# Kernel optimization log

Hardware: AMD Instinct MI355X
Metric: run time of the kernel (lower is better)

Reference implementation:

```python
import jax, jax.numpy as jnp
import numpy as np

N, C, T, V, O, S, R = 32, 64, 256, 25, 192, 3, 8  # batch, in_ch, time, joints, out_ch, subsets, rel_ch


def setup_inputs() -> dict:
    key = jax.random.key(0)
    ks = jax.random.split(key, 20)
    w = lambda i, shape: (jax.random.normal(ks[i], shape, jnp.float32) * 0.05)
    return {
        "x": jax.random.normal(ks[0], (N, C, T, V), jnp.float32),
        "spd_A": jax.random.normal(ks[1], (V, V), jnp.float32) * 0.1,
        "A3": jax.random.normal(ks[2], (S, V, V), jnp.float32) * 0.1,
        "A6": jax.random.normal(ks[3], (6, V, V), jnp.float32) * 0.1,
        "conv1_w": w(4, (S, R, C)), "conv1_b": jnp.zeros((S, R), jnp.float32),
        "conv2_w": w(5, (S, R, C)), "conv2_b": jnp.zeros((S, R), jnp.float32),
        "conv4_w": w(6, (S, O, R)), "conv4_b": jnp.zeros((S, O), jnp.float32),
        "conv3_w": w(7, (S, O, C)), "conv3_b": jnp.zeros((S, O), jnp.float32),
        "alpha": jnp.full((1,), 0.5, jnp.float32),
        "beta": jnp.full((1,), 0.5, jnp.float32),
        "gamma": jnp.full((1,), 0.5, jnp.float32),
        "bn_w": jnp.ones((O,), jnp.float32), "bn_b": jnp.zeros((O,), jnp.float32),
        "down_w": w(8, (O, C)), "down_b": jnp.zeros((O,), jnp.float32),
        "dbn_w": jnp.ones((O,), jnp.float32), "dbn_b": jnp.zeros((O,), jnp.float32),
    }


def _bn(y, w, b):
    # BatchNorm2d in training mode: stats over (N, T, V) per channel, biased var
    mu = y.mean(axis=(0, 2, 3), keepdims=True)
    var = ((y - mu) ** 2).mean(axis=(0, 2, 3), keepdims=True)
    return (y - mu) * jax.lax.rsqrt(var + 1e-5) * w[None, :, None, None] + b[None, :, None, None]


def reference(x, spd_A, A3, A6, conv1_w, conv1_b, conv2_w, conv2_b, conv4_w, conv4_b,
              conv3_w, conv3_b, alpha, beta, gamma, bn_w, bn_b, down_w, down_b, dbn_w, dbn_b):
    out_c = conv4_w.shape[1]
    # A6 expanded: (out//6, 6, V, V) -> (out, V, V); contiguous-view == tile along channel blocks
    A6_ex = jnp.tile(A6, (out_c // 6, 1, 1))  # (O, V, V)
    # 1x1 conv then temporal mean == conv on temporal mean (linear op commutes)
    xm = x.mean(axis=2)  # (N, C, V)
    x1 = jnp.einsum('ncv,src->nsrv', xm, conv1_w) + conv1_b[None, :, :, None]
    x2 = jnp.einsum('ncv,src->nsrv', xm, conv2_w) + conv2_b[None, :, :, None]
    d = jnp.tanh(x1[..., :, None] - x2[..., None, :])  # (N, S, R, V, V)
    A_dyn = jnp.einsum('nsruv,sor->nsouv', d, conv4_w) + conv4_b[None, :, :, None, None]
    A_at = (A_dyn * alpha + A3[None, :, None, :, :]
            + A6_ex[None, None] * beta + spd_A[None, None, None] * gamma)  # (N, S, O, V, V)
    # CTRGC_2: x3 = conv3(x); einsum 'ncuv,nctv->nctu', summed over subsets
    x3 = jnp.einsum('nctv,soc->nsotv', x, conv3_w) + conv3_b[None, :, :, None, None]
    y = jnp.einsum('nsouv,nsotv->notu', A_at, x3)  # (N, O, T, V)
    y = _bn(y, bn_w, bn_b)
    xd = jnp.einsum('nctv,oc->notv', x, down_w) + down_b[None, :, None, None]
    y = jax.nn.relu(y + _bn(xd, dbn_w, dbn_b))
    return y
```

## Files before the change

### kernel.cpp

```cpp
#include <hip/hip_runtime.h>

#define N_ 32
#define C_ 64
#define T_ 256
#define V_ 25
#define O_ 192
#define S_ 3
#define R_ 8
#define VV (V_*V_)
#define TV (T_*V_)
#define RP 26
#define TRP (T_*RP)

typedef unsigned short u16;
typedef unsigned int u32;
typedef __attribute__((ext_vector_type(4))) u16 u16x4;
typedef __attribute__((ext_vector_type(8))) u16 u16x8;
typedef __attribute__((ext_vector_type(4))) u32 u32x4;
typedef __attribute__((ext_vector_type(8))) __bf16 bf16x8;
typedef __attribute__((ext_vector_type(4))) float f32x4;

#define WS_A2F_U 0
#define WS_XQ_U  (18874368)
#define WS_XD_U  (18874368 + 13631488)
#define WS_XM_F   (35913728)
#define WS_RS_F   (35913728 + 51200)
#define WS_STAT_F (35913728 + 51200 + 153600)
#define WS_COEF_F (35913728 + 51200 + 153600 + 768)

__device__ __forceinline__ u16 f2b(float f) {
    return __builtin_bit_cast(u16, (__bf16)f);
}
__device__ __forceinline__ float b2f(u16 u) {
    return __builtin_bit_cast(float, ((unsigned)u) << 16);
}
__device__ __forceinline__ f32x4 mfma16(bf16x8 a, bf16x8 b, f32x4 c) {
    return __builtin_amdgcn_mfma_f32_16x16x32_bf16(a, b, c, 0, 0, 0);
}

__global__ void k0_xq(const float* __restrict__ x, u16* __restrict__ xq) {
    __shared__ float tile[64][52];
    int bid = blockIdx.x;
    int n = bid >> 7, tb = bid & 127;
    int t0 = tb * 2;
    int tid = threadIdx.x;
    const float2* xp = (const float2*)(x + (size_t)n * C_ * TV + t0 * 25);
    for (int p = tid; p < 1600; p += 256) {
        int c = p / 25, q = p % 25;
        float2 f2 = xp[(size_t)c * 3200 + q];
        tile[c][q * 2] = f2.x;
        tile[c][q * 2 + 1] = f2.y;
    }
    __syncthreads();
    for (int p = tid; p < 832; p += 256) {
        int row = p >> 4, c4g = p & 15;
        int t = row >= RP, v = row - t * RP;
        u16x4 w;
        #pragma unroll
        for (int i = 0; i < 4; ++i) {
            int co = ((c4g & 3) << 4) + ((c4g >> 2) << 2) + i;
            w[i] = (v < 25) ? f2b(tile[co][t * 25 + v]) : (u16)0;
        }
        *(u16x4*)&xq[((size_t)n * TRP + tb * 52 + row) * 64 + c4g * 4] = w;
    }
}

__global__ void k1_xm(const float* __restrict__ x, float* __restrict__ xm_out) {
    __shared__ float ps[256];
    int nc = blockIdx.x;
    int tid = threadIdx.x;
    const float* xp = x + (size_t)nc * TV;
    float acc = 0.f;
    if (tid < 250) {
        int tg = tid / 25, v = tid % 25;
        for (int j = 0; j < 26; ++j) {
            int t = tg + 10 * j;
            if (t < T_) acc += xp[t * V_ + v];
        }
    }
    ps[tid] = acc;
    __syncthreads();
    if (tid < V_) {
        float s = 0.f;
        for (int tg = 0; tg < 10; ++tg) s += ps[tg * 25 + tid];
        xm_out[(size_t)nc * V_ + tid] = s * (1.f / T_);
    }
}

__global__ void k2_a2f(const float* __restrict__ spd, const float* __restrict__ A3,
                       const float* __restrict__ A6,
                       const float* __restrict__ w1, const float* __restrict__ b1,
                       const float* __restrict__ w2, const float* __restrict__ b2,
                       const float* __restrict__ w4, const float* __restrict__ b4,
                       const float* __restrict__ b3,
                       const float* __restrict__ alpha, const float* __restrict__ beta,
                       const float* __restrict__ gamma,
                       u16* __restrict__ a2f, const float* __restrict__ xmbuf,
                       float* __restrict__ rs_tot) {
    __shared__ float xm[C_ * V_];
    __shared__ float x1s[R_ * V_], x2s[R_ * V_];
    __shared__ float dm[R_ * VV];
    __shared__ float a3s[VV], sps[VV], a6s[6 * VV];
    __shared__ float aat[2 * VV];
    __shared__ float w4s[2][R_];
    __shared__ float b4s[2];
    int bid = blockIdx.x;
    int n = bid / 24;
    int rem = bid % 24;
    int s = rem / 8, og = rem % 8;
    int tid = threadIdx.x;
    const float* xmg = xmbuf + (size_t)n * C_ * V_;
    for (int p = tid; p < C_ * V_; p += 256) xm[p] = xmg[p];
    for (int p = tid; p < VV; p += 256) { a3s[p] = A3[s * VV + p]; sps[p] = spd[p]; }
    for (int p = tid; p < 6 * VV; p += 256) a6s[p] = A6[p];
    __syncthreads();
    if (tid < R_ * V_) {
        int r = tid / V_, v = tid % V_;
        float acc1 = b1[s * R_ + r], acc2 = b2[s * R_ + r];
        for (int c = 0; c < C_; ++c) {
            float xv = xm[c * V_ + v];
            acc1 += xv * w1[(s * R_ + r) * C_ + c];
            acc2 += xv * w2[(s * R_ + r) * C_ + c];
        }
        x1s[tid] = acc1; x2s[tid] = acc2;
    }
    __syncthreads();
    for (int p = tid; p < R_ * VV; p += 256) {
        int r = p / VV, uv = p % VV, u = uv / V_, v = uv % V_;
        dm[p] = tanhf(x1s[r * V_ + u] - x2s[r * V_ + v]);
    }
    __syncthreads();
    float al = alpha[0], be = beta[0], ga = gamma[0];
    for (int op = 0; op < 12; ++op) {
        int o0 = og * 24 + op * 2;
        if (tid < 16) w4s[tid >> 3][tid & 7] =
            w4[((size_t)(s * O_ + o0 + (tid >> 3))) * R_ + (tid & 7)];
        if (tid < 2) b4s[tid] = b4[s * O_ + o0 + tid];
        __syncthreads();
        for (int p = tid; p < 2 * VV; p += 256) {
            int oo = p / VV, pp = p % VV;
            float acc = b4s[oo];
            #pragma unroll
            for (int r = 0; r < R_; ++r) acc += dm[r * VV + pp] * w4s[oo][r];
            int o = o0 + oo;
            aat[p] = al * acc + a3s[pp] + be * a6s[(o % 6) * VV + pp] + ga * sps[pp];
        }
        __syncthreads();
        if (tid < 2 * V_) {
            int oo = tid / V_, u = tid % V_;
            float rs = 0.f;
            for (int v = 0; v < V_; ++v) rs += aat[oo * VV + u * V_ + v];
            atomicAdd(&rs_tot[((size_t)(n * O_ + o0 + oo)) * V_ + u],
                      b3[s * O_ + o0 + oo] * rs);
        }
        {
            int oo = tid >> 7, l2 = tid & 127, cu = l2 >> 6, l = l2 & 63;
            int u = cu * 16 + (l & 15);
            u16x8 w;
            #pragma unroll
            for (int j = 0; j < 8; ++j) {
                int v = ((j >> 2) << 4) + ((l >> 4) << 2) + (j & 3);
                float val = 0.f;
                if (u < V_ && v < V_) val = aat[oo * VV + u * V_ + v];
                w[j] = f2b(val);
            }
            size_t idx = ((((size_t)(n * O_ + o0 + oo)) * S_ + s) * 2 + cu) * 64 + l;
            ((u16x8*)a2f)[idx] = w;
        }
        __syncthreads();
    }
}

#define OSTR_B 2504
#define SSTR_B 832
#define BUF_B  20096

__global__ __launch_bounds__(256, 3)
void k3_main(const u16* __restrict__ xq,
             const float* __restrict__ w3, const float* __restrict__ dw,
             const float* __restrict__ db,
             const u16* __restrict__ a2f, const float* __restrict__ rs_tot,
             float* __restrict__ yout, u16* __restrict__ xdws,
             float* __restrict__ stats) {
    __shared__ char x3Lb[2 * BUF_B];
    int orig = blockIdx.x;
    int bid = (orig & 7) * 96 + (orig >> 3);
    int n = bid / 24;
    int o0 = (bid % 24) * 8;
    int tid = threadIdx.x, wid = tid >> 6, lane = tid & 63;
    int lr = lane & 15, lg = lane >> 4;
    int colt = wid & 1;
    int rt0 = (wid >> 1) * 13;

    for (int p = tid; p < 2 * BUF_B / 16; p += 256) ((u32x4*)x3Lb)[p] = u32x4{0,0,0,0};

    const float* wsrc = (colt == 0)
        ? w3 + ((size_t)((lr >> 3) * O_ + o0 + (lr & 7))) * C_
        : ((lr < 8) ? w3 + ((size_t)(2 * O_ + o0 + lr)) * C_
                    : dw + ((size_t)(o0 + lr - 8)) * C_);
    bf16x8 bw[2];
    #pragma unroll
    for (int ks = 0; ks < 2; ++ks) {
        u16x8 tmp;
        #pragma unroll
        for (int j = 0; j < 8; ++j) {
            int c = ks * 32 + (lg << 2) + (j & 3) + ((j >> 2) << 4);
            tmp[j] = f2b(wsrc[c]);
        }
        bw[ks] = __builtin_bit_cast(bf16x8, tmp);
    }
    float dbv = (colt == 1 && lr >= 8) ? db[o0 + lr - 8] : 0.f;

    int wo = (colt == 0) ? (lr & 7) : lr;
    int wsb = (colt == 0) ? (lr >> 3) : 2;
    int colbyte = wo * OSTR_B + wsb * SSTR_B;

    const bf16x8* a2v = (const bf16x8*)a2f;
    bf16x8 Bh[2][6];
    float rsb0[2], rsb1[2];
    #pragma unroll
    for (int oi = 0; oi < 2; ++oi) {
        int o = o0 + (wid << 1) + oi;
        const bf16x8* bp = a2v + ((size_t)(n * O_ + o)) * 6 * 64 + lane;
        #pragma unroll
        for (int q = 0; q < 6; ++q) Bh[oi][q] = bp[(size_t)q * 64];
        const float* rsp = rs_tot + ((size_t)(n * O_ + o)) * V_;
        rsb0[oi] = rsp[lr];
        rsb1[oi] = (lr < 9) ? rsp[16 + lr] : 0.f;
    }

    float sy1[2] = {0, 0}, sy2[2] = {0, 0};
    float sd1 = 0.f, sd2 = 0.f;
    const u16* xbn = xq + (size_t)n * TRP * 64;
    int rdw = 13 * lr + 2 * lg;
    __syncthreads();

    for (int ch = 0; ch < 16; ++ch) {
        int t0 = ch * 16;
        char* buf = x3Lb + (ch & 1) * BUF_B;
        const u16* xrow = xbn + (size_t)t0 * RP * 64;
        for (int rt = rt0; rt < rt0 + 13; ++rt) {
            const u16* ap = xrow + (size_t)(rt * 16 + lr) * 64 + (lg << 4);
            u16x8 A0 = *(const u16x8*)ap;
            u16x8 A1 = *(const u16x8*)(ap + 8);
            f32x4 acc = {0.f, 0.f, 0.f, 0.f};
            acc = mfma16(__builtin_bit_cast(bf16x8, A0), bw[0], acc);
            acc = mfma16(__builtin_bit_cast(bf16x8, A1), bw[1], acc);
            int rbase = rt * 16 + (lg << 2);
            if (colt == 0 || lr < 8) {
                u16x4 w;
                #pragma unroll
                for (int reg = 0; reg < 4; ++reg) w[reg] = f2b(acc[reg]);
                *(u16x4*)(buf + colbyte + rbase * 2) = w;
            } else {
                size_t xdb = ((size_t)(n * O_ + o0 + lr - 8)) * TV + (size_t)t0 * V_;
                #pragma unroll
                for (int reg = 0; reg < 4; ++reg) {
                    int rr = rbase + reg;
                    int t = rr / RP, v = rr - t * RP;
                    if (v < 25) {
                        float val = acc[reg] + dbv;
                        xdws[xdb + t * V_ + v] = f2b(val);
                        sd1 += val; sd2 += val * val;
                    }
                }
            }
        }
        __syncthreads();
        #pragma unroll
        for (int oi = 0; oi < 2; ++oi) {
            int ol = (wid << 1) + oi;
            int o = o0 + ol;
            const u32* L = (const u32*)(buf + ol * OSTR_B);
            f32x4 acc0 = {0, 0, 0, 0}, acc1 = {0, 0, 0, 0};
            #pragma unroll
            for (int s = 0; s < 3; ++s) {
                const u32* Ls = L + s * 208 + rdw;
                u32 d0 = Ls[0], d1 = Ls[1], d8 = Ls[8], d9 = Ls[9];
                bf16x8 A = __builtin_bit_cast(bf16x8, u32x4{d0, d1, d8, d9});
                acc0 = mfma16(A, Bh[oi][s * 2 + 0], acc0);
                acc1 = mfma16(A, Bh[oi][s * 2 + 1], acc1);
            }
            size_t yb = ((size_t)(n * O_ + o) * T_ + t0 + (lg << 2)) * V_;
            #pragma unroll
            for (int reg = 0; reg < 4; ++reg) {
                float v0 = acc0[reg] + rsb0[oi];
                yout[yb + (size_t)reg * V_ + lr] = v0;
                sy1[oi] += v0; sy2[oi] += v0 * v0;
                if (lr < 9) {
                    float v1 = acc1[reg] + rsb1[oi];
                    yout[yb + (size_t)reg * V_ + 16 + lr] = v1;
                    sy1[oi] += v1; sy2[oi] += v1 * v1;
                }
            }
        }
    }
    #pragma unroll
    for (int oi = 0; oi < 2; ++oi) {
        float v1 = sy1[oi], v2 = sy2[oi];
        #pragma unroll
        for (int m = 1; m < 64; m <<= 1) {
            v1 += __shfl_xor(v1, m);
            v2 += __shfl_xor(v2, m);
        }
        if (lane == 0) {
            atomicAdd(&stats[0 * O_ + o0 + (wid << 1) + oi], v1);
            atomicAdd(&stats[1 * O_ + o0 + (wid << 1) + oi], v2);
        }
    }
    if (colt == 1) {
        float v1 = sd1, v2 = sd2;
        v1 += __shfl_xor(v1, 16); v2 += __shfl_xor(v2, 16);
        v1 += __shfl_xor(v1, 32); v2 += __shfl_xor(v2, 32);
        if (lane >= 8 && lane < 16) {
            atomicAdd(&stats[2 * O_ + o0 + lane - 8], v1);
            atomicAdd(&stats[3 * O_ + o0 + lane - 8], v2);
        }
    }
}

__global__ void k4_coef(const float* __restrict__ bn_w, const float* __restrict__ bn_b,
                        const float* __restrict__ dbn_w, const float* __restrict__ dbn_b,
                        const float* __restrict__ stats, float* __restrict__ coef) {
    int o = threadIdx.x;
    if (o >= O_) return;
    float inv = 1.f / (float)(N_ * T_ * V_);
    float mu_y = stats[o] * inv;
    float var_y = stats[O_ + o] * inv - mu_y * mu_y;
    float ay = bn_w[o] * rsqrtf(var_y + 1e-5f);
    float by = bn_b[o] - mu_y * ay;
    float mu_d = stats[2 * O_ + o] * inv;
    float var_d = stats[3 * O_ + o] * inv - mu_d * mu_d;
    float ad = dbn_w[o] * rsqrtf(var_d + 1e-5f);
    float bd = dbn_b[o] - mu_d * ad;
    coef[o] = ay; coef[O_ + o] = by; coef[2 * O_ + o] = ad; coef[3 * O_ + o] = bd;
}

__global__ void k5_final(float* __restrict__ out, const u16* __restrict__ xd,
                         const float* __restrict__ cf) {
    size_t total = (size_t)N_ * O_ * TV / 8;
    for (size_t i = blockIdx.x * (size_t)blockDim.x + threadIdx.x; i < total;
         i += (size_t)gridDim.x * blockDim.x) {
        int o = (int)((i / 800) % O_);
        float ay = cf[o], by = cf[O_ + o], ad = cf[2 * O_ + o], bd = cf[3 * O_ + o];
        float4 y0 = ((float4*)out)[2 * i];
        float4 y1 = ((float4*)out)[2 * i + 1];
        u16x8 dv = ((const u16x8*)xd)[i];
        float4 r0, r1;
        r0.x = fmaxf(ay * y0.x + by + ad * b2f(dv[0]) + bd, 0.f);
        r0.y = fmaxf(ay * y0.y + by + ad * b2f(dv[1]) + bd, 0.f);
        r0.z = fmaxf(ay * y0.z + by + ad * b2f(dv[2]) + bd, 0.f);
        r0.w = fmaxf(ay * y0.w + by + ad * b2f(dv[3]) + bd, 0.f);
        r1.x = fmaxf(ay * y1.x + by + ad * b2f(dv[4]) + bd, 0.f);
        r1.y = fmaxf(ay * y1.y + by + ad * b2f(dv[5]) + bd, 0.f);
        r1.z = fmaxf(ay * y1.z + by + ad * b2f(dv[6]) + bd, 0.f);
        r1.w = fmaxf(ay * y1.w + by + ad * b2f(dv[7]) + bd, 0.f);
        ((float4*)out)[2 * i] = r0;
        ((float4*)out)[2 * i + 1] = r1;
    }
}

extern "C" void kernel_launch(void* const* d_in, const int* in_sizes, int n_in,
                              void* d_out, int out_size, void* d_ws, size_t ws_size,
                              hipStream_t stream) {
    const float* x     = (const float*)d_in[0];
    const float* spd   = (const float*)d_in[1];
    const float* A3    = (const float*)d_in[2];
    const float* A6    = (const float*)d_in[3];
    const float* w1    = (const float*)d_in[4];
    const float* b1    = (const float*)d_in[5];
    const float* w2    = (const float*)d_in[6];
    const float* b2    = (const float*)d_in[7];
    const float* w4    = (const float*)d_in[8];
    const float* b4    = (const float*)d_in[9];
    const float* w3    = (const float*)d_in[10];
    const float* b3    = (const float*)d_in[11];
    const float* alpha = (const float*)d_in[12];
    const float* beta  = (const float*)d_in[13];
    const float* gamma = (const float*)d_in[14];
    const float* bn_w  = (const float*)d_in[15];
    const float* bn_b  = (const float*)d_in[16];
    const float* dw    = (const float*)d_in[17];
    const float* db    = (const float*)d_in[18];
    const float* dbn_w = (const float*)d_in[19];
    const float* dbn_b = (const float*)d_in[20];
    float* out = (float*)d_out;
    u16*   wsu = (u16*)d_ws;
    float* wsf = (float*)d_ws;

    u16* a2f  = wsu + WS_A2F_U;
    u16* xq   = wsu + WS_XQ_U;
    u16* xd   = wsu + WS_XD_U;
    float* xm    = wsf + WS_XM_F;
    float* rs    = wsf + WS_RS_F;
    float* stats = wsf + WS_STAT_F;
    float* coef  = wsf + WS_COEF_F;

    hipMemsetAsync(rs, 0, (N_ * O_ * V_ + 4 * O_) * sizeof(float), stream);

    k0_xq<<<N_ * 128, 256, 0, stream>>>(x, xq);
    k1_xm<<<N_ * C_, 256, 0, stream>>>(x, xm);
    k2_a2f<<<N_ * S_ * 8, 256, 0, stream>>>(spd, A3, A6, w1, b1, w2, b2, w4, b4, b3,
                                            alpha, beta, gamma, a2f, xm, rs);
    k3_main<<<N_ * 24, 256, 0, stream>>>(xq, w3, dw, db, a2f, rs, out, xd, stats);
    k4_coef<<<1, 256, 0, stream>>>(bn_w, bn_b, dbn_w, dbn_b, stats, coef);
    k5_final<<<4096, 256, 0, stream>>>(out, xd, coef);
}
```

Baseline: 366.3 us.

## Store pre-BN output as bf16 via LDS staging, fuse temporal mean into k0

The main kernel now writes its pre-normalization output y as bf16 into a workspace buffer instead of fp32 into the output tensor. Both y and the downsample branch are staged in shared memory so global writes become coalesced 16-byte stores rather than scattered 2- and 4-byte stores. The final kernel reads bf16 y instead of fp32, and the separate temporal-mean kernel is folded into k0 using atomic adds into a zeroed buffer. This cuts global write and read traffic and drops a launch, at the cost of extra LDS use, more atomics, and lower precision for the intermediate y.

New measurement: 335.3 us. 1.09x faster.

```diff
diff --git a/kernel.cpp b/kernel.cpp
--- a/kernel.cpp
+++ b/kernel.cpp
@@ -23,10 +23,11 @@
 #define WS_A2F_U 0
 #define WS_XQ_U  (18874368)
 #define WS_XD_U  (18874368 + 13631488)
-#define WS_XM_F   (35913728)
-#define WS_RS_F   (35913728 + 51200)
-#define WS_STAT_F (35913728 + 51200 + 153600)
-#define WS_COEF_F (35913728 + 51200 + 153600 + 768)
+#define WS_YB_U  (18874368 + 13631488 + 39321600)
+#define WS_XM_F   (55574528)
+#define WS_RS_F   (55574528 + 51200)
+#define WS_STAT_F (55574528 + 51200 + 153600)
+#define WS_COEF_F (55574528 + 51200 + 153600 + 768)
 
 __device__ __forceinline__ u16 f2b(float f) {
     return __builtin_bit_cast(u16, (__bf16)f);
@@ -38,7 +39,8 @@
     return __builtin_amdgcn_mfma_f32_16x16x32_bf16(a, b, c, 0, 0, 0);
 }
 
-__global__ void k0_xq(const float* __restrict__ x, u16* __restrict__ xq) {
+__global__ void k0_xq(const float* __restrict__ x, u16* __restrict__ xq,
+                      float* __restrict__ xm) {
     __shared__ float tile[64][52];
     int bid = blockIdx.x;
     int n = bid >> 7, tb = bid & 127;
@@ -63,27 +65,10 @@
         }
         *(u16x4*)&xq[((size_t)n * TRP + tb * 52 + row) * 64 + c4g * 4] = w;
     }
-}
-
-__global__ void k1_xm(const float* __restrict__ x, float* __restrict__ xm_out) {
-    __shared__ float ps[256];
-    int nc = blockIdx.x;
-    int tid = threadIdx.x;
-    const float* xp = x + (size_t)nc * TV;
-    float acc = 0.f;
-    if (tid < 250) {
-        int tg = tid / 25, v = tid % 25;
-        for (int j = 0; j < 26; ++j) {
-            int t = tg + 10 * j;
-            if (t < T_) acc += xp[t * V_ + v];
-        }
-    }
-    ps[tid] = acc;
-    __syncthreads();
-    if (tid < V_) {
-        float s = 0.f;
-        for (int tg = 0; tg < 10; ++tg) s += ps[tg * 25 + tid];
-        xm_out[(size_t)nc * V_ + tid] = s * (1.f / T_);
+    for (int p = tid; p < 1600; p += 256) {
+        int c = p / 25, v = p % 25;
+        float s = (tile[c][v] + tile[c][25 + v]) * (1.f / T_);
+        atomicAdd(&xm[((size_t)n * C_ + c) * V_ + v], s);
     }
 }
 
@@ -173,16 +158,18 @@
 
 #define OSTR_B 2504
 #define SSTR_B 832
-#define BUF_B  20096
+#define BUF_B  20064
 
 __global__ __launch_bounds__(256, 3)
 void k3_main(const u16* __restrict__ xq,
              const float* __restrict__ w3, const float* __restrict__ dw,
              const float* __restrict__ db,
              const u16* __restrict__ a2f, const float* __restrict__ rs_tot,
-             float* __restrict__ yout, u16* __restrict__ xdws,
+             u16* __restrict__ yb16, u16* __restrict__ xdws,
              float* __restrict__ stats) {
     __shared__ char x3Lb[2 * BUF_B];
+    __shared__ u16 xdst[8 * 416];
+    __shared__ u16 ystage[8 * 400];
     int orig = blockIdx.x;
     int bid = (orig & 7) * 96 + (orig >> 3);
     int n = bid / 24;
@@ -253,24 +240,22 @@
                 for (int reg = 0; reg < 4; ++reg) w[reg] = f2b(acc[reg]);
                 *(u16x4*)(buf + colbyte + rbase * 2) = w;
             } else {
-                size_t xdb = ((size_t)(n * O_ + o0 + lr - 8)) * TV + (size_t)t0 * V_;
+                u16x4 w;
                 #pragma unroll
                 for (int reg = 0; reg < 4; ++reg) {
                     int rr = rbase + reg;
                     int t = rr / RP, v = rr - t * RP;
-                    if (v < 25) {
-                        float val = acc[reg] + dbv;
-                        xdws[xdb + t * V_ + v] = f2b(val);
-                        sd1 += val; sd2 += val * val;
-                    }
+                    float val = acc[reg] + dbv;
+                    w[reg] = f2b(val);
+                    if (v < 25) { sd1 += val; sd2 += val * val; }
                 }
+                *(u16x4*)&xdst[(lr - 8) * 416 + rbase] = w;
             }
         }
         __syncthreads();
         #pragma unroll
         for (int oi = 0; oi < 2; ++oi) {
             int ol = (wid << 1) + oi;
-            int o = o0 + ol;
             const u32* L = (const u32*)(buf + ol * OSTR_B);
             f32x4 acc0 = {0, 0, 0, 0}, acc1 = {0, 0, 0, 0};
             #pragma unroll
@@ -281,17 +266,43 @@
                 acc0 = mfma16(A, Bh[oi][s * 2 + 0], acc0);
                 acc1 = mfma16(A, Bh[oi][s * 2 + 1], acc1);
             }
-            size_t yb = ((size_t)(n * O_ + o) * T_ + t0 + (lg << 2)) * V_;
+            int ylb = ol * 400 + (lg << 2) * 25;
             #pragma unroll
             for (int reg = 0; reg < 4; ++reg) {
                 float v0 = acc0[reg] + rsb0[oi];
-                yout[yb + (size_t)reg * V_ + lr] = v0;
+                ystage[ylb + reg * 25 + lr] = f2b(v0);
                 sy1[oi] += v0; sy2[oi] += v0 * v0;
                 if (lr < 9) {
                     float v1 = acc1[reg] + rsb1[oi];
-                    yout[yb + (size_t)reg * V_ + 16 + lr] = v1;
+                    ystage[ylb + reg * 25 + 16 + lr] = f2b(v1);
                     sy1[oi] += v1; sy2[oi] += v1 * v1;
                 }
+            }
+        }
+        {
+            size_t ygb = (size_t)(n * O_ + o0) * TV + (size_t)t0 * V_;
+            for (int q = lane; q < 100; q += 64) {
+                int sel = q >= 50;
+                int ol2 = (wid << 1) + sel;
+                int j = q - sel * 50;
+                u16x8 pk = *(const u16x8*)&ystage[ol2 * 400 + j * 8];
+                *(u16x8*)&yb16[ygb + (size_t)ol2 * TV + j * 8] = pk;
+            }
+        }
+        if (colt == 1) {
+            int tofs = (wid >> 1) * 8;
+            size_t gdb = (size_t)(n * O_ + o0) * TV + (size_t)(t0 + tofs) * V_;
+            for (int q = lane; q < 200; q += 64) {
+                int o = q / 25, w = q - o * 25;
+                int g0 = w * 8;
+                int tl = g0 / 25, v = g0 - tl * 25;
+                u16x8 pk;
+                #pragma unroll
+                for (int k = 0; k < 8; ++k) {
+                    pk[k] = xdst[o * 416 + (tofs + tl) * RP + v];
+                    if (++v == 25) { v = 0; ++tl; }
+                }
+                *(u16x8*)&xdws[gdb + (size_t)o * TV + g0] = pk;
             }
         }
     }
@@ -336,25 +347,24 @@
     coef[o] = ay; coef[O_ + o] = by; coef[2 * O_ + o] = ad; coef[3 * O_ + o] = bd;
 }
 
-__global__ void k5_final(float* __restrict__ out, const u16* __restrict__ xd,
-                         const float* __restrict__ cf) {
+__global__ void k5_final(float* __restrict__ out, const u16* __restrict__ yb,
+                         const u16* __restrict__ xd, const float* __restrict__ cf) {
     size_t total = (size_t)N_ * O_ * TV / 8;
     for (size_t i = blockIdx.x * (size_t)blockDim.x + threadIdx.x; i < total;
          i += (size_t)gridDim.x * blockDim.x) {
         int o = (int)((i / 800) % O_);
         float ay = cf[o], by = cf[O_ + o], ad = cf[2 * O_ + o], bd = cf[3 * O_ + o];
-        float4 y0 = ((float4*)out)[2 * i];
-        float4 y1 = ((float4*)out)[2 * i + 1];
+        u16x8 yv = ((const u16x8*)yb)[i];
         u16x8 dv = ((const u16x8*)xd)[i];
         float4 r0, r1;
-        r0.x = fmaxf(ay * y0.x + by + ad * b2f(dv[0]) + bd, 0.f);
-        r0.y = fmaxf(ay * y0.y + by + ad * b2f(dv[1]) + bd, 0.f);
-        r0.z = fmaxf(ay * y0.z + by + ad * b2f(dv[2]) + bd, 0.f);
-        r0.w = fmaxf(ay * y0.w + by + ad * b2f(dv[3]) + bd, 0.f);
-        r1.x = fmaxf(ay * y1.x + by + ad * b2f(dv[4]) + bd, 0.f);
-        r1.y = fmaxf(ay * y1.y + by + ad * b2f(dv[5]) + bd, 0.f);
-        r1.z = fmaxf(ay * y1.z + by + ad * b2f(dv[6]) + bd, 0.f);
-        r1.w = fmaxf(ay * y1.w + by + ad * b2f(dv[7]) + bd, 0.f);
+        r0.x = fmaxf(ay * b2f(yv[0]) + by + ad * b2f(dv[0]) + bd, 0.f);
+        r0.y = fmaxf(ay * b2f(yv[1]) + by + ad * b2f(dv[1]) + bd, 0.f);
+        r0.z = fmaxf(ay * b2f(yv[2]) + by + ad * b2f(dv[2]) + bd, 0.f);
+        r0.w = fmaxf(ay * b2f(yv[3]) + by + ad * b2f(dv[3]) + bd, 0.f);
+        r1.x = fmaxf(ay * b2f(yv[4]) + by + ad * b2f(dv[4]) + bd, 0.f);
+        r1.y = fmaxf(ay * b2f(yv[5]) + by + ad * b2f(dv[5]) + bd, 0.f);
+        r1.z = fmaxf(ay * b2f(yv[6]) + by + ad * b2f(dv[6]) + bd, 0.f);
+        r1.w = fmaxf(ay * b2f(yv[7]) + by + ad * b2f(dv[7]) + bd, 0.f);
         ((float4*)out)[2 * i] = r0;
         ((float4*)out)[2 * i + 1] = r1;
     }
@@ -391,18 +401,19 @@
     u16* a2f  = wsu + WS_A2F_U;
     u16* xq   = wsu + WS_XQ_U;
     u16* xd   = wsu + WS_XD_U;
+    u16* yb   = wsu + WS_YB_U;
     float* xm    = wsf + WS_XM_F;
     float* rs    = wsf + WS_RS_F;
     float* stats = wsf + WS_STAT_F;
     float* coef  = wsf + WS_COEF_F;
 
-    hipMemsetAsync(rs, 0, (N_ * O_ * V_ + 4 * O_) * sizeof(float), stream);
-
-    k0_xq<<<N_ * 128, 256, 0, stream>>>(x, xq);
-    k1_xm<<<N_ * C_, 256, 0, stream>>>(x, xm);
+    hipMemsetAsync(xm, 0, (N_ * C_ * V_ + N_ * O_ * V_ + 4 * O_) * sizeof(float),
+                   stream);
+
+    k0_xq<<<N_ * 128, 256, 0, stream>>>(x, xq, xm);
     k2_a2f<<<N_ * S_ * 8, 256, 0, stream>>>(spd, A3, A6, w1, b1, w2, b2, w4, b4, b3,
                                             alpha, beta, gamma, a2f, xm, rs);
-    k3_main<<<N_ * 24, 256, 0, stream>>>(xq, w3, dw, db, a2f, rs, out, xd, stats);
+    k3_main<<<N_ * 24, 256, 0, stream>>>(xq, w3, dw, db, a2f, rs, yb, xd, stats);
     k4_coef<<<1, 256, 0, stream>>>(bn_w, bn_b, dbn_w, dbn_b, stats, coef);
-    k5_final<<<4096, 256, 0, stream>>>(out, xd, coef);
-}
+    k5_final<<<4096, 256, 0, stream>>>(out, yb, xd, coef);
+}
```
